# Kernel tuning notes

Hardware: AMD Instinct MI355X
Metric: run time of the kernel (lower is better)

## Reference

```python
import jax, jax.numpy as jnp
import numpy as np

D_MODEL = 1024
N_HEADS = 16
D_HEAD = D_MODEL // N_HEADS
WINDOW = 128
D_FF = 3 * D_MODEL
EPS = 1e-5


def _layer_norm(x, g, b):
    mu = jnp.mean(x, axis=-1, keepdims=True)
    var = jnp.var(x, axis=-1, keepdims=True)
    return (x - mu) * jax.lax.rsqrt(var + EPS) * g + b


def setup_inputs() -> dict:
    key = jax.random.key(0)
    ks = jax.random.split(key, 10)
    B, S = 2, 2048
    sd = 0.02
    return {
        "x": jax.random.normal(ks[0], (B, S, D_MODEL), dtype=jnp.float32),
        "w_qkv": jax.random.normal(ks[1], (D_MODEL, 3 * D_MODEL), dtype=jnp.float32) * sd,
        "b_qkv": jnp.zeros((3 * D_MODEL,), jnp.float32),
        "w_out": jax.random.normal(ks[2], (D_MODEL, D_MODEL), dtype=jnp.float32) * sd,
        "b_out": jnp.zeros((D_MODEL,), jnp.float32),
        "w_ff1": jax.random.normal(ks[3], (D_MODEL, D_FF), dtype=jnp.float32) * sd,
        "b_ff1": jnp.zeros((D_FF,), jnp.float32),
        "w_ff2": jax.random.normal(ks[4], (D_FF, D_MODEL), dtype=jnp.float32) * sd,
        "b_ff2": jnp.zeros((D_MODEL,), jnp.float32),
        "ln1_g": jnp.ones((D_MODEL,), jnp.float32),
        "ln1_b": jnp.zeros((D_MODEL,), jnp.float32),
        "ln2_g": jnp.ones((D_MODEL,), jnp.float32),
        "ln2_b": jnp.zeros((D_MODEL,), jnp.float32),
    }


def reference(x, w_qkv, b_qkv, w_out, b_out, w_ff1, b_ff1, w_ff2, b_ff2,
              ln1_g, ln1_b, ln2_g, ln2_b):
    B, S, D = x.shape
    h = _layer_norm(x, ln1_g, ln1_b)
    qkv = (h @ w_qkv + b_qkv).reshape(B, S, 3, N_HEADS, D_HEAD)
    q, k, v = (jnp.moveaxis(qkv[:, :, i], 1, 2) for i in range(3))  # (B,H,S,dh)
    scores = jnp.einsum('bhqd,bhkd->bhqk', q, k) / jnp.sqrt(jnp.float32(D_HEAD))
    i = jnp.arange(S)[:, None]
    j = jnp.arange(S)[None, :]
    allowed = (j <= i) & (j > i - WINDOW)  # causal sliding window band
    scores = jnp.where(allowed, scores, -jnp.inf)
    attn = jax.nn.softmax(scores, axis=-1)
    ctx = jnp.einsum('bhqk,bhkd->bqhd', attn, v).reshape(B, S, D)
    x = x + (ctx @ w_out + b_out)
    h2 = _layer_norm(x, ln2_g, ln2_b)
    ff = jax.nn.gelu(h2 @ w_ff1 + b_ff1, approximate=False) @ w_ff2 + b_ff2
    return x + ff
```

## Files before the change

kernel.cpp:

```cpp
#include <hip/hip_runtime.h>

#define D_MODEL 1024
#define SEQ 2048
#define BATCH 2
#define NH 16
#define DH 64
#define WIN 128
#define DFF 3072

typedef __bf16 bf16x8 __attribute__((ext_vector_type(8)));
typedef float f32x4 __attribute__((ext_vector_type(4)));
typedef unsigned short u16;
typedef unsigned int u32;

__device__ __forceinline__ float b2f(u16 u) {
    unsigned int x = ((unsigned int)u) << 16;
    return __uint_as_float(x);
}
__device__ __forceinline__ u16 f2b(float f) {
    unsigned int x = __float_as_uint(f);
    x += 0x7fffu + ((x >> 16) & 1u);
    return (u16)(x >> 16);
}
__device__ __forceinline__ u32 pk2(float a, float b) {
    return (u32)f2b(a) | ((u32)f2b(b) << 16);
}

#define WAIT_VMCNT0() __builtin_amdgcn_s_waitcnt(0x0F70)

__global__ __launch_bounds__(256) void prep_k(
        const float* __restrict__ x, const float* __restrict__ g1,
        const float* __restrict__ bt1, u16* __restrict__ hbf,
        const float* __restrict__ wqkv, u16* __restrict__ wqkvT,
        const float* __restrict__ wout, u16* __restrict__ woutT,
        const float* __restrict__ wff1, u16* __restrict__ wff1T,
        const float* __restrict__ wff2, u16* __restrict__ wff2T) {
    __shared__ u16 tile[64][65];
    __shared__ float s1[4], s2[4];
    int bid = blockIdx.x;
    int tid = threadIdx.x;
    if (bid < 2560) {
        const float* in; u16* out; int R, C, loc, gx;
        if (bid < 768)       { in = wqkv; out = wqkvT; R = 1024; C = 3072; loc = bid;        gx = 48; }
        else if (bid < 1024) { in = wout; out = woutT; R = 1024; C = 1024; loc = bid - 768;  gx = 16; }
        else if (bid < 1792) { in = wff1; out = wff1T; R = 1024; C = 3072; loc = bid - 1024; gx = 48; }
        else                 { in = wff2; out = wff2T; R = 3072; C = 1024; loc = bid - 1792; gx = 16; }
        int bx = loc % gx, by = loc / gx;
        int r0 = by * 64, c0 = bx * 64;
        int w = tid >> 6, cc = tid & 63;
#pragma unroll
        for (int i = 0; i < 16; ++i) {
            int r = i * 4 + w;
            tile[r][cc] = f2b(in[(size_t)(r0 + r) * C + c0 + cc]);
        }
        __syncthreads();
        int rr = (tid & 15) * 4;
        int cb = tid >> 4;
#pragma unroll
        for (int j = 0; j < 4; ++j) {
            int c = cb + j * 16;
            ushort4 p = {tile[rr][c], tile[rr + 1][c],
                         tile[rr + 2][c], tile[rr + 3][c]};
            *(ushort4*)&out[(size_t)(c0 + c) * R + r0 + rr] = p;
        }
    } else {
        int row = bid - 2560;
        const float* xr = x + (size_t)row * D_MODEL;
        float v[4];
        float sum = 0.f, sq = 0.f;
#pragma unroll
        for (int i = 0; i < 4; ++i) {
            v[i] = xr[tid + i * 256];
            sum += v[i];
            sq += v[i] * v[i];
        }
#pragma unroll
        for (int off = 32; off > 0; off >>= 1) {
            sum += __shfl_xor(sum, off, 64);
            sq  += __shfl_xor(sq, off, 64);
        }
        int w = tid >> 6;
        if ((tid & 63) == 0) { s1[w] = sum; s2[w] = sq; }
        __syncthreads();
        sum = s1[0] + s1[1] + s1[2] + s1[3];
        sq  = s2[0] + s2[1] + s2[2] + s2[3];
        float mu = sum * (1.f / D_MODEL);
        float var = sq * (1.f / D_MODEL) - mu * mu;
        float rstd = rsqrtf(var + 1e-5f);
        u16* outr = hbf + (size_t)row * D_MODEL;
#pragma unroll
        for (int i = 0; i < 4; ++i) {
            int c = tid + i * 256;
            outr[c] = f2b((v[i] - mu) * rstd * g1[c] + bt1[c]);
        }
    }
}

__global__ __launch_bounds__(256) void ln_k(
        const float* __restrict__ x, const float* __restrict__ g,
        const float* __restrict__ bta, u16* __restrict__ out) {
    int row = blockIdx.x;
    const float* xr = x + (size_t)row * D_MODEL;
    float v[4];
    float sum = 0.f, sq = 0.f;
#pragma unroll
    for (int i = 0; i < 4; ++i) {
        v[i] = xr[threadIdx.x + i * 256];
        sum += v[i];
        sq += v[i] * v[i];
    }
#pragma unroll
    for (int off = 32; off > 0; off >>= 1) {
        sum += __shfl_xor(sum, off, 64);
        sq  += __shfl_xor(sq, off, 64);
    }
    __shared__ float s1[4], s2[4];
    int w = threadIdx.x >> 6;
    if ((threadIdx.x & 63) == 0) { s1[w] = sum; s2[w] = sq; }
    __syncthreads();
    sum = s1[0] + s1[1] + s1[2] + s1[3];
    sq  = s2[0] + s2[1] + s2[2] + s2[3];
    float mu = sum * (1.f / D_MODEL);
    float var = sq * (1.f / D_MODEL) - mu * mu;
    float rstd = rsqrtf(var + 1e-5f);
    u16* outr = out + (size_t)row * D_MODEL;
#pragma unroll
    for (int i = 0; i < 4; ++i) {
        int c = threadIdx.x + i * 256;
        outr[c] = f2b((v[i] - mu) * rstd * g[c] + bta[c]);
    }
}

template <int GELU, int VSPLIT>
__global__ __launch_bounds__(256, 3) void gemm3_k(
        const u16* __restrict__ A, const u16* __restrict__ Bt,
        const float* __restrict__ bias, u16* __restrict__ Cb,
        u16* __restrict__ vt, int M, int N, int K, int ldc) {
    __shared__ u16 As[2 * 128 * 64];
    __shared__ u16 Bs[2 * 64 * 64];
    int tid = threadIdx.x;
    int w = tid >> 6, lane = tid & 63;
    int qd = lane >> 4, l15 = lane & 15;

    int lin = blockIdx.x;
    int xcd = lin & 7, idx = lin >> 3;
    int m0 = (xcd * 4 + (idx & 3)) * 128;
    int n0 = (idx >> 2) * 64;

    const u16* gsrc[6];
    u16* ldst[6];
    int nboff[6];
#pragma unroll
    for (int i = 0; i < 6; ++i) {
        int c = w * 6 + i;
        int isA = c < 16;
        int cb = isA ? c : c - 16;
        int row = cb * 8 + (lane >> 3);
        int cg = (lane & 7) ^ (row & 7);
        gsrc[i] = (isA ? A + (size_t)(m0 + row) * K
                       : Bt + (size_t)(n0 + row) * K) + cg * 8;
        ldst[i] = (isA ? As : Bs) + cb * 512;
        nboff[i] = isA ? 8192 : 4096;
    }

    int wm = w & 1, wn = w >> 1;
    f32x4 acc[4][2];
#pragma unroll
    for (int mt = 0; mt < 4; ++mt)
#pragma unroll
        for (int nt = 0; nt < 2; ++nt)
            acc[mt][nt] = (f32x4){0.f, 0.f, 0.f, 0.f};

    int aoff[4][2], boff[2][2];
#pragma unroll
    for (int t = 0; t < 4; ++t) {
        int ar = wm * 64 + t * 16 + l15;
#pragma unroll
        for (int h = 0; h < 2; ++h)
            aoff[t][h] = ar * 64 + (((h * 4 + qd) ^ (ar & 7)) * 8);
    }
#pragma unroll
    for (int t = 0; t < 2; ++t) {
        int br = wn * 32 + t * 16 + l15;
#pragma unroll
        for (int h = 0; h < 2; ++h)
            boff[t][h] = br * 64 + (((h * 4 + qd) ^ (br & 7)) * 8);
    }

#pragma unroll
    for (int i = 0; i < 6; ++i)
        __builtin_amdgcn_global_load_lds(
            (__attribute__((address_space(1))) void*)(gsrc[i]),
            (__attribute__((address_space(3))) void*)(ldst[i]), 16, 0, 0);

    int nsteps = K >> 6;

#define TSTEP3(S, RB)                                                       \
    {                                                                       \
        WAIT_VMCNT0();                                                      \
        __builtin_amdgcn_s_barrier();                                       \
        if ((S) + 1 < nsteps) {                                             \
            int k0 = ((S) + 1) << 6;                                        \
            _Pragma("unroll")                                               \
            for (int i = 0; i < 6; ++i)                                     \
                __builtin_amdgcn_global_load_lds(                           \
                    (__attribute__((address_space(1))) void*)(gsrc[i] + k0),\
                    (__attribute__((address_space(3))) void*)(ldst[i] +     \
                        (1 - (RB)) * nboff[i]),                             \
                    16, 0, 0);                                              \
        }                                                                   \
        bf16x8 av[4][2], bv[2][2];                                          \
        _Pragma("unroll")                                                   \
        for (int t = 0; t < 4; ++t)                                         \
            _Pragma("unroll")                                               \
            for (int h = 0; h < 2; ++h)                                     \
                av[t][h] = *(const bf16x8*)&As[aoff[t][h] + (RB) * 8192];   \
        _Pragma("unroll")                                                   \
        for (int t = 0; t < 2; ++t)                                         \
            _Pragma("unroll")                                               \
            for (int h = 0; h < 2; ++h)                                     \
                bv[t][h] = *(const bf16x8*)&Bs[boff[t][h] + (RB) * 4096];   \
        _Pragma("unroll")                                                   \
        for (int mt = 0; mt < 4; ++mt)                                      \
            _Pragma("unroll")                                               \
            for (int nt = 0; nt < 2; ++nt) {                                \
                acc[mt][nt] = __builtin_amdgcn_mfma_f32_16x16x32_bf16(      \
                    av[mt][0], bv[nt][0], acc[mt][nt], 0, 0, 0);            \
                acc[mt][nt] = __builtin_amdgcn_mfma_f32_16x16x32_bf16(      \
                    av[mt][1], bv[nt][1], acc[mt][nt], 0, 0, 0);            \
            }                                                               \
    }

    for (int s = 0; s < nsteps; s += 2) {
        TSTEP3(s, 0);
        TSTEP3(s + 1, 1);
    }

#pragma unroll
    for (int mt = 0; mt < 4; ++mt) {
        int row0 = m0 + wm * 64 + mt * 16 + qd * 4;
#pragma unroll
        for (int nt = 0; nt < 2; ++nt) {
            int col = n0 + wn * 32 + nt * 16 + l15;
            float v[4];
#pragma unroll
            for (int reg = 0; reg < 4; ++reg) {
                v[reg] = acc[mt][nt][reg] + bias[col];
                if (GELU) v[reg] = 0.5f * v[reg] * (1.f + erff(v[reg] * 0.70710678118654752f));
            }
            if (VSPLIT && col >= 2 * D_MODEL) {
                int d = col - 2 * D_MODEL;
                int bh = (row0 >> 11) * NH + (d >> 6);
                ushort4 pkv = {f2b(v[0]), f2b(v[1]), f2b(v[2]), f2b(v[3])};
                *(ushort4*)&vt[((size_t)(bh * DH + (d & 63))) * SEQ + (row0 & (SEQ - 1))] = pkv;
            } else {
#pragma unroll
                for (int reg = 0; reg < 4; ++reg)
                    Cb[(size_t)(row0 + reg) * ldc + col] = f2b(v[reg]);
            }
        }
    }
}

__global__ __launch_bounds__(256, 3) void gemm_tall_k(
        const u16* __restrict__ A, const u16* __restrict__ Bt,
        const float* __restrict__ bias, const float* __restrict__ resid,
        float* __restrict__ C, int M, int N, int K, int ldc) {
    __shared__ u16 As[2 * 64 * 64];
    __shared__ u16 Bs[2 * 128 * 64];
    int tid = threadIdx.x;
    int w = tid >> 6, lane = tid & 63;
    int qd = lane >> 4, l15 = lane & 15;

    int lin = blockIdx.x;
    int xcd = lin & 7, idx = lin >> 3;
    int m0 = (xcd * 8 + (idx & 7)) * 64;
    int n0 = (idx >> 3) * 128;

    const u16* gsrc[6];
    u16* ldst[6];
    int nboff[6];
#pragma unroll
    for (int i = 0; i < 6; ++i) {
        int c = w * 6 + i;
        int isA = c < 8;
        int cb = isA ? c : c - 8;
        int row = cb * 8 + (lane >> 3);
        int cg = (lane & 7) ^ (row & 7);
        gsrc[i] = (isA ? A + (size_t)(m0 + row) * K
                       : Bt + (size_t)(n0 + row) * K) + cg * 8;
        ldst[i] = (isA ? As : Bs) + cb * 512;
        nboff[i] = isA ? 4096 : 8192;
    }

    int wm = w & 1, wn = w >> 1;
    f32x4 acc[2][4];
#pragma unroll
    for (int mt = 0; mt < 2; ++mt)
#pragma unroll
        for (int nt = 0; nt < 4; ++nt)
            acc[mt][nt] = (f32x4){0.f, 0.f, 0.f, 0.f};

    int aoff[2][2], boff[4][2];
#pragma unroll
    for (int t = 0; t < 2; ++t) {
        int ar = wm * 32 + t * 16 + l15;
#pragma unroll
        for (int h = 0; h < 2; ++h)
            aoff[t][h] = ar * 64 + (((h * 4 + qd) ^ (ar & 7)) * 8);
    }
#pragma unroll
    for (int t = 0; t < 4; ++t) {
        int br = wn * 64 + t * 16 + l15;
#pragma unroll
        for (int h = 0; h < 2; ++h)
            boff[t][h] = br * 64 + (((h * 4 + qd) ^ (br & 7)) * 8);
    }

#pragma unroll
    for (int i = 0; i < 6; ++i)
        __builtin_amdgcn_global_load_lds(
            (__attribute__((address_space(1))) void*)(gsrc[i]),
            (__attribute__((address_space(3))) void*)(ldst[i]), 16, 0, 0);

    int nsteps = K >> 6;

#define TSTEP64(S, RB)                                                      \
    {                                                                       \
        WAIT_VMCNT0();                                                      \
        __builtin_amdgcn_s_barrier();                                       \
        if ((S) + 1 < nsteps) {                                             \
            int k0 = ((S) + 1) << 6;                                        \
            _Pragma("unroll")                                               \
            for (int i = 0; i < 6; ++i)                                     \
                __builtin_amdgcn_global_load_lds(                           \
                    (__attribute__((address_space(1))) void*)(gsrc[i] + k0),\
                    (__attribute__((address_space(3))) void*)(ldst[i] +     \
                        (1 - (RB)) * nboff[i]),                             \
                    16, 0, 0);                                              \
        }                                                                   \
        bf16x8 av[2][2], bv[4][2];                                          \
        _Pragma("unroll")                                                   \
        for (int t = 0; t < 2; ++t)                                         \
            _Pragma("unroll")                                               \
            for (int h = 0; h < 2; ++h)                                     \
                av[t][h] = *(const bf16x8*)&As[aoff[t][h] + (RB) * 4096];   \
        _Pragma("unroll")                                                   \
        for (int t = 0; t < 4; ++t)                                         \
            _Pragma("unroll")                                               \
            for (int h = 0; h < 2; ++h)                                     \
                bv[t][h] = *(const bf16x8*)&Bs[boff[t][h] + (RB) * 8192];   \
        _Pragma("unroll")                                                   \
        for (int mt = 0; mt < 2; ++mt)                                      \
            _Pragma("unroll")                                               \
            for (int nt = 0; nt < 4; ++nt) {                                \
                acc[mt][nt] = __builtin_amdgcn_mfma_f32_16x16x32_bf16(      \
                    av[mt][0], bv[nt][0], acc[mt][nt], 0, 0, 0);            \
                acc[mt][nt] = __builtin_amdgcn_mfma_f32_16x16x32_bf16(      \
                    av[mt][1], bv[nt][1], acc[mt][nt], 0, 0, 0);            \
            }                                                               \
    }

    for (int s = 0; s < nsteps; s += 2) {
        TSTEP64(s, 0);
        TSTEP64(s + 1, 1);
    }

#pragma unroll
    for (int mt = 0; mt < 2; ++mt) {
        int row0 = m0 + wm * 32 + mt * 16 + qd * 4;
#pragma unroll
        for (int nt = 0; nt < 4; ++nt) {
            int col = n0 + wn * 64 + nt * 16 + l15;
#pragma unroll
            for (int reg = 0; reg < 4; ++reg) {
                float v = acc[mt][nt][reg] + bias[col]
                        + resid[(size_t)(row0 + reg) * ldc + col];
                C[(size_t)(row0 + reg) * ldc + col] = v;
            }
        }
    }
}

__global__ __launch_bounds__(256) void attn_k(
        const u16* __restrict__ qk, const u16* __restrict__ vt,
        u16* __restrict__ ctx) {
    int lane = threadIdx.x & 63, l15 = lane & 15, quad = lane >> 4;
    int t = blockIdx.x * 4 + (threadIdx.x >> 6);
    int qt = t & (SEQ / 16 - 1);
    int h  = (t >> 7) & (NH - 1);
    int b  = t >> 11;
    int q0 = qt * 16;
    int bh = b * NH + h;

    const u16* qrow = qk + (size_t)(b * SEQ + q0 + l15) * (2 * D_MODEL) + h * DH + quad * 8;
    bf16x8 qf0 = *(const bf16x8*)(qrow);
    bf16x8 qf1 = *(const bf16x8*)(qrow + 32);
    const u16* kbase = qk + (size_t)(b * SEQ) * (2 * D_MODEL) + D_MODEL + h * DH + quad * 8;
    const u16* vbase = vt + (size_t)(bh * DH) * SEQ;

    f32x4 o[4] = {{0.f, 0.f, 0.f, 0.f}, {0.f, 0.f, 0.f, 0.f},
                  {0.f, 0.f, 0.f, 0.f}, {0.f, 0.f, 0.f, 0.f}};
    float m = -1e30f, l = 0.f;
    int q = q0 + l15;
    int cs = q0 - (WIN - 1);
    cs = cs < 0 ? 0 : (cs & ~31);

    for (int c = cs; c <= q0 + 15; c += 32) {
        const u16* k0p = kbase + (size_t)(c + l15) * (2 * D_MODEL);
        const u16* k1p = k0p + (size_t)16 * (2 * D_MODEL);
        bf16x8 ka0 = *(const bf16x8*)(k0p);
        bf16x8 ka1 = *(const bf16x8*)(k0p + 32);
        bf16x8 kb0 = *(const bf16x8*)(k1p);
        bf16x8 kb1 = *(const bf16x8*)(k1p + 32);
        f32x4 s0 = {0.f, 0.f, 0.f, 0.f}, s1 = {0.f, 0.f, 0.f, 0.f};
        s0 = __builtin_amdgcn_mfma_f32_16x16x32_bf16(ka0, qf0, s0, 0, 0, 0);
        s0 = __builtin_amdgcn_mfma_f32_16x16x32_bf16(ka1, qf1, s0, 0, 0, 0);
        s1 = __builtin_amdgcn_mfma_f32_16x16x32_bf16(kb0, qf0, s1, 0, 0, 0);
        s1 = __builtin_amdgcn_mfma_f32_16x16x32_bf16(kb1, qf1, s1, 0, 0, 0);

        float p0[4], p1[4];
        float cm = -1e30f;
#pragma unroll
        for (int reg = 0; reg < 4; ++reg) {
            int k0i = c + quad * 4 + reg;
            p0[reg] = ((unsigned)(q - k0i) < WIN) ? s0[reg] * 0.125f : -1e30f;
            p1[reg] = ((unsigned)(q - k0i - 16) < WIN) ? s1[reg] * 0.125f : -1e30f;
            cm = fmaxf(cm, fmaxf(p0[reg], p1[reg]));
        }
        cm = fmaxf(cm, __shfl_xor(cm, 16, 64));
        cm = fmaxf(cm, __shfl_xor(cm, 32, 64));
        float mn = fmaxf(m, cm);
        float alpha = __expf(m - mn);
        m = mn;
        float ls = 0.f;
#pragma unroll
        for (int reg = 0; reg < 4; ++reg) {
            p0[reg] = __expf(p0[reg] - mn);
            p1[reg] = __expf(p1[reg] - mn);
            ls += p0[reg] + p1[reg];
        }
        ls += __shfl_xor(ls, 16, 64);
        ls += __shfl_xor(ls, 32, 64);
        l = l * alpha + ls;
#pragma unroll
        for (int mt = 0; mt < 4; ++mt) o[mt] *= alpha;

        u32 z0 = pk2(p0[0], p0[1]), z1 = pk2(p0[2], p0[3]);
        u32 w0 = pk2(p1[0], p1[1]), w1 = pk2(p1[2], p1[3]);
        int slo = ((quad & 1) * 2) * 16 + l15;
        int shi = slo + 16;
        u32 zl0 = (u32)__shfl((int)z0, slo, 64), zl1 = (u32)__shfl((int)z1, slo, 64);
        u32 zh0 = (u32)__shfl((int)z0, shi, 64), zh1 = (u32)__shfl((int)z1, shi, 64);
        u32 wl0 = (u32)__shfl((int)w0, slo, 64), wl1 = (u32)__shfl((int)w1, slo, 64);
        u32 wh0 = (u32)__shfl((int)w0, shi, 64), wh1 = (u32)__shfl((int)w1, shi, 64);
        alignas(16) u32 pr[4];
        pr[0] = quad < 2 ? zl0 : wl0;
        pr[1] = quad < 2 ? zl1 : wl1;
        pr[2] = quad < 2 ? zh0 : wh0;
        pr[3] = quad < 2 ? zh1 : wh1;
        bf16x8 pf = *(const bf16x8*)pr;

#pragma unroll
        for (int mt = 0; mt < 4; ++mt) {
            bf16x8 vf = *(const bf16x8*)(vbase + (size_t)(mt * 16 + l15) * SEQ + c + quad * 8);
            o[mt] = __builtin_amdgcn_mfma_f32_16x16x32_bf16(vf, pf, o[mt], 0, 0, 0);
        }
    }

    float rdiv = 1.f / l;
    u16* crow = ctx + (size_t)(b * SEQ + q0 + l15) * D_MODEL + h * DH;
#pragma unroll
    for (int mt = 0; mt < 4; ++mt) {
        ushort4 pkv = {f2b(o[mt][0] * rdiv), f2b(o[mt][1] * rdiv),
                       f2b(o[mt][2] * rdiv), f2b(o[mt][3] * rdiv)};
        *(ushort4*)(crow + mt * 16 + quad * 4) = pkv;
    }
}

extern "C" void kernel_launch(void* const* d_in, const int* in_sizes, int n_in,
                              void* d_out, int out_size, void* d_ws, size_t ws_size,
                              hipStream_t stream) {
    (void)in_sizes; (void)n_in; (void)out_size; (void)ws_size;
    const float* x     = (const float*)d_in[0];
    const float* w_qkv = (const float*)d_in[1];
    const float* b_qkv = (const float*)d_in[2];
    const float* w_out = (const float*)d_in[3];
    const float* b_out = (const float*)d_in[4];
    const float* w_ff1 = (const float*)d_in[5];
    const float* b_ff1 = (const float*)d_in[6];
    const float* w_ff2 = (const float*)d_in[7];
    const float* b_ff2 = (const float*)d_in[8];
    const float* ln1g  = (const float*)d_in[9];
    const float* ln1b  = (const float*)d_in[10];
    const float* ln2g  = (const float*)d_in[11];
    const float* ln2b  = (const float*)d_in[12];
    float* out = (float*)d_out;

    const int M = BATCH * SEQ;
    char* base = (char*)d_ws;
    u16*   hbf   = (u16*)(base);
    u16*   qkbuf = (u16*)(base + (8ll  << 20));
    u16*   ctxbf = (u16*)(base + (24ll << 20));
    u16*   vtbuf = (u16*)(base + (32ll << 20));
    u16*   ffbf  = (u16*)(base + (8ll  << 20));
    float* x2    = (float*)(base + (40ll << 20));
    u16*   wqkvT = (u16*)(base + (56ll << 20));
    u16*   woutT = (u16*)(base + (62ll << 20));
    u16*   wff1T = (u16*)(base + (64ll << 20));
    u16*   wff2T = (u16*)(base + (70ll << 20));

    prep_k<<<dim3(6656), 256, 0, stream>>>(
        x, ln1g, ln1b, hbf, w_qkv, wqkvT, w_out, woutT,
        w_ff1, wff1T, w_ff2, wff2T);
    gemm3_k<0, 1><<<dim3((M / 128) * (3 * D_MODEL / 64)), 256, 0, stream>>>(
        hbf, wqkvT, b_qkv, qkbuf, vtbuf, M, 3 * D_MODEL, D_MODEL, 2 * D_MODEL);
    attn_k<<<dim3(BATCH * NH * (SEQ / 16) / 4), 256, 0, stream>>>(qkbuf, vtbuf, ctxbf);
    gemm_tall_k<<<dim3(512), 256, 0, stream>>>(
        ctxbf, woutT, b_out, x, x2, M, D_MODEL, D_MODEL, D_MODEL);
    ln_k<<<M, 256, 0, stream>>>(x2, ln2g, ln2b, hbf);
    gemm3_k<1, 0><<<dim3((M / 128) * (DFF / 64)), 256, 0, stream>>>(
        hbf, wff1T, b_ff1, ffbf, nullptr, M, DFF, D_MODEL, DFF);
    gemm_tall_k<<<dim3(512), 256, 0, stream>>>(
        ffbf, wff2T, b_ff2, x2, out, M, D_MODEL, DFF, D_MODEL);
}
```

Before: 268.0 us.

## Single-buffer GEMM LDS to raise occupancy and vectorize layernorm loads

The GEMM kernel drops its double-buffered LDS pipeline in favour of a single buffer with load, wait, compute and barrier each k-step, and raises the launch-bounds occupancy hint from 3 to 6 blocks. The aim is to hide memory latency through more resident waves instead of software prefetch. The cost is that loads and MFMA work within a block no longer overlap, and a second barrier is added per step. Separately, both layernorm paths switch to float4 loads and ushort4 stores so each thread handles four contiguous elements.

```diff
diff --git a/kernel.cpp b/kernel.cpp
--- a/kernel.cpp
+++ b/kernel.cpp
@@ -65,15 +65,9 @@
         }
     } else {
         int row = bid - 2560;
-        const float* xr = x + (size_t)row * D_MODEL;
-        float v[4];
-        float sum = 0.f, sq = 0.f;
-#pragma unroll
-        for (int i = 0; i < 4; ++i) {
-            v[i] = xr[tid + i * 256];
-            sum += v[i];
-            sq += v[i] * v[i];
-        }
+        float4 v = ((const float4*)(x + (size_t)row * D_MODEL))[tid];
+        float sum = v.x + v.y + v.z + v.w;
+        float sq  = v.x * v.x + v.y * v.y + v.z * v.z + v.w * v.w;
 #pragma unroll
         for (int off = 32; off > 0; off >>= 1) {
             sum += __shfl_xor(sum, off, 64);
@@ -87,12 +81,13 @@
         float mu = sum * (1.f / D_MODEL);
         float var = sq * (1.f / D_MODEL) - mu * mu;
         float rstd = rsqrtf(var + 1e-5f);
-        u16* outr = hbf + (size_t)row * D_MODEL;
-#pragma unroll
-        for (int i = 0; i < 4; ++i) {
-            int c = tid + i * 256;
-            outr[c] = f2b((v[i] - mu) * rstd * g1[c] + bt1[c]);
-        }
+        float4 gg = ((const float4*)g1)[tid];
+        float4 bb = ((const float4*)bt1)[tid];
+        ushort4 o = {f2b((v.x - mu) * rstd * gg.x + bb.x),
+                     f2b((v.y - mu) * rstd * gg.y + bb.y),
+                     f2b((v.z - mu) * rstd * gg.z + bb.z),
+                     f2b((v.w - mu) * rstd * gg.w + bb.w)};
+        *(ushort4*)&hbf[(size_t)row * D_MODEL + tid * 4] = o;
     }
 }
 
@@ -100,44 +95,40 @@
         const float* __restrict__ x, const float* __restrict__ g,
         const float* __restrict__ bta, u16* __restrict__ out) {
     int row = blockIdx.x;
-    const float* xr = x + (size_t)row * D_MODEL;
-    float v[4];
-    float sum = 0.f, sq = 0.f;
-#pragma unroll
-    for (int i = 0; i < 4; ++i) {
-        v[i] = xr[threadIdx.x + i * 256];
-        sum += v[i];
-        sq += v[i] * v[i];
-    }
+    int tid = threadIdx.x;
+    float4 v = ((const float4*)(x + (size_t)row * D_MODEL))[tid];
+    float sum = v.x + v.y + v.z + v.w;
+    float sq  = v.x * v.x + v.y * v.y + v.z * v.z + v.w * v.w;
 #pragma unroll
     for (int off = 32; off > 0; off >>= 1) {
         sum += __shfl_xor(sum, off, 64);
         sq  += __shfl_xor(sq, off, 64);
     }
     __shared__ float s1[4], s2[4];
-    int w = threadIdx.x >> 6;
-    if ((threadIdx.x & 63) == 0) { s1[w] = sum; s2[w] = sq; }
+    int w = tid >> 6;
+    if ((tid & 63) == 0) { s1[w] = sum; s2[w] = sq; }
     __syncthreads();
     sum = s1[0] + s1[1] + s1[2] + s1[3];
     sq  = s2[0] + s2[1] + s2[2] + s2[3];
     float mu = sum * (1.f / D_MODEL);
     float var = sq * (1.f / D_MODEL) - mu * mu;
     float rstd = rsqrtf(var + 1e-5f);
-    u16* outr = out + (size_t)row * D_MODEL;
-#pragma unroll
-    for (int i = 0; i < 4; ++i) {
-        int c = threadIdx.x + i * 256;
-        outr[c] = f2b((v[i] - mu) * rstd * g[c] + bta[c]);
-    }
+    float4 gg = ((const float4*)g)[tid];
+    float4 bb = ((const float4*)bta)[tid];
+    ushort4 o = {f2b((v.x - mu) * rstd * gg.x + bb.x),
+                 f2b((v.y - mu) * rstd * gg.y + bb.y),
+                 f2b((v.z - mu) * rstd * gg.z + bb.z),
+                 f2b((v.w - mu) * rstd * gg.w + bb.w)};
+    *(ushort4*)&out[(size_t)row * D_MODEL + tid * 4] = o;
 }
 
 template <int GELU, int VSPLIT>
-__global__ __launch_bounds__(256, 3) void gemm3_k(
+__global__ __launch_bounds__(256, 6) void gemm3_k(
         const u16* __restrict__ A, const u16* __restrict__ Bt,
         const float* __restrict__ bias, u16* __restrict__ Cb,
         u16* __restrict__ vt, int M, int N, int K, int ldc) {
-    __shared__ u16 As[2 * 128 * 64];
-    __shared__ u16 Bs[2 * 64 * 64];
+    __shared__ u16 As[128 * 64];
+    __shared__ u16 Bs[64 * 64];
     int tid = threadIdx.x;
     int w = tid >> 6, lane = tid & 63;
     int qd = lane >> 4, l15 = lane & 15;
@@ -149,7 +140,6 @@
 
     const u16* gsrc[6];
     u16* ldst[6];
-    int nboff[6];
 #pragma unroll
     for (int i = 0; i < 6; ++i) {
         int c = w * 6 + i;
@@ -160,7 +150,6 @@
         gsrc[i] = (isA ? A + (size_t)(m0 + row) * K
                        : Bt + (size_t)(n0 + row) * K) + cg * 8;
         ldst[i] = (isA ? As : Bs) + cb * 512;
-        nboff[i] = isA ? 8192 : 4096;
     }
 
     int wm = w & 1, wn = w >> 1;
@@ -187,53 +176,37 @@
             boff[t][h] = br * 64 + (((h * 4 + qd) ^ (br & 7)) * 8);
     }
 
-#pragma unroll
-    for (int i = 0; i < 6; ++i)
-        __builtin_amdgcn_global_load_lds(
-            (__attribute__((address_space(1))) void*)(gsrc[i]),
-            (__attribute__((address_space(3))) void*)(ldst[i]), 16, 0, 0);
-
     int nsteps = K >> 6;
-
-#define TSTEP3(S, RB)                                                       \
-    {                                                                       \
-        WAIT_VMCNT0();                                                      \
-        __builtin_amdgcn_s_barrier();                                       \
-        if ((S) + 1 < nsteps) {                                             \
-            int k0 = ((S) + 1) << 6;                                        \
-            _Pragma("unroll")                                               \
-            for (int i = 0; i < 6; ++i)                                     \
-                __builtin_amdgcn_global_load_lds(                           \
-                    (__attribute__((address_space(1))) void*)(gsrc[i] + k0),\
-                    (__attribute__((address_space(3))) void*)(ldst[i] +     \
-                        (1 - (RB)) * nboff[i]),                             \
-                    16, 0, 0);                                              \
-        }                                                                   \
-        bf16x8 av[4][2], bv[2][2];                                          \
-        _Pragma("unroll")                                                   \
-        for (int t = 0; t < 4; ++t)                                         \
-            _Pragma("unroll")                                               \
-            for (int h = 0; h < 2; ++h)                                     \
-                av[t][h] = *(const bf16x8*)&As[aoff[t][h] + (RB) * 8192];   \
-        _Pragma("unroll")                                                   \
-        for (int t = 0; t < 2; ++t)                                         \
-            _Pragma("unroll")                                               \
-            for (int h = 0; h < 2; ++h)                                     \
-                bv[t][h] = *(const bf16x8*)&Bs[boff[t][h] + (RB) * 4096];   \
-        _Pragma("unroll")                                                   \
-        for (int mt = 0; mt < 4; ++mt)                                      \
-            _Pragma("unroll")                                               \
-            for (int nt = 0; nt < 2; ++nt) {                                \
-                acc[mt][nt] = __builtin_amdgcn_mfma_f32_16x16x32_bf16(      \
-                    av[mt][0], bv[nt][0], acc[mt][nt], 0, 0, 0);            \
-                acc[mt][nt] = __builtin_amdgcn_mfma_f32_16x16x32_bf16(      \
-                    av[mt][1], bv[nt][1], acc[mt][nt], 0, 0, 0);            \
-            }                                                               \
-    }
-
-    for (int s = 0; s < nsteps; s += 2) {
-        TSTEP3(s, 0);
-        TSTEP3(s + 1, 1);
+    for (int s = 0; s < nsteps; ++s) {
+        int k0 = s << 6;
+#pragma unroll
+        for (int i = 0; i < 6; ++i)
+            __builtin_amdgcn_global_load_lds(
+                (__attribute__((address_space(1))) void*)(gsrc[i] + k0),
+                (__attribute__((address_space(3))) void*)(ldst[i]), 16, 0, 0);
+        WAIT_VMCNT0();
+        __builtin_amdgcn_s_barrier();
+        bf16x8 av[4][2], bv[2][2];
+#pragma unroll
+        for (int t = 0; t < 4; ++t)
+#pragma unroll
+            for (int h = 0; h < 2; ++h)
+                av[t][h] = *(const bf16x8*)&As[aoff[t][h]];
+#pragma unroll
+        for (int t = 0; t < 2; ++t)
+#pragma unroll
+            for (int h = 0; h < 2; ++h)
+                bv[t][h] = *(const bf16x8*)&Bs[boff[t][h]];
+#pragma unroll
+        for (int mt = 0; mt < 4; ++mt)
+#pragma unroll
+            for (int nt = 0; nt < 2; ++nt) {
+                acc[mt][nt] = __builtin_amdgcn_mfma_f32_16x16x32_bf16(
+                    av[mt][0], bv[nt][0], acc[mt][nt], 0, 0, 0);
+                acc[mt][nt] = __builtin_amdgcn_mfma_f32_16x16x32_bf16(
+                    av[mt][1], bv[nt][1], acc[mt][nt], 0, 0, 0);
+            }
+        __builtin_amdgcn_s_barrier();
     }
 
 #pragma unroll
```

Measured after the change: 273.8 us. 2.2% more time.
